# Kernel tuning notes

Measured on AMD Instinct MI355X. Metric: run time of the kernel, lower is better.

The kernel has to match this reference:

```python
import jax, jax.numpy as jnp
import numpy as np

BATCH, IN_DIM, OUT_DIM = 4096, 8192, 16384

# Each of the 16 logic gates is affine in {1, a, b, a*b}. Rows below give the
# coefficients (const, a, b, ab) for gate k, matching the torch `gate` match-case.
_GATE_COEFS = np.array([
    [0, 0, 0, 0],    # 0: zeros
    [0, 0, 0, 1],    # 1: a*b
    [0, 1, 0, -1],   # 2: a - a*b
    [0, 1, 0, 0],    # 3: a
    [0, 0, 1, -1],   # 4: b - a*b
    [0, 0, 1, 0],    # 5: b
    [0, 1, 1, -2],   # 6: a + b - 2ab (xor)
    [0, 1, 1, -1],   # 7: a + b - ab (or)
    [1, -1, -1, 1],  # 8: 1 - (a + b - ab) (nor)
    [1, -1, -1, 2],  # 9: 1 - (a + b - 2ab) (xnor)
    [1, 0, -1, 0],   # 10: 1 - b
    [1, 0, -1, 1],   # 11: 1 - b + ab
    [1, -1, 0, 0],   # 12: 1 - a
    [1, -1, 0, 1],   # 13: 1 - a + ab
    [1, 0, 0, -1],   # 14: 1 - ab (nand)
    [1, 0, 0, 0],    # 15: ones
], dtype=np.float32)


def setup_inputs() -> dict:
    key = jax.random.key(0)
    k1, k2, k3, k4 = jax.random.split(key, 4)
    x = jax.random.uniform(k1, (BATCH, IN_DIM), dtype=jnp.float32)
    weights = jax.random.normal(k2, (OUT_DIM, 16), dtype=jnp.float32)
    idx_a = jax.random.randint(k3, (OUT_DIM,), 0, IN_DIM, dtype=jnp.int32)
    idx_b = jax.random.randint(k4, (OUT_DIM,), 0, IN_DIM, dtype=jnp.int32)
    return {"x": x, "weights": weights, "idx_a": idx_a, "idx_b": idx_b}


def reference(x, weights, idx_a, idx_b):
    # Training path: softmax over the 16 gate logits per output neuron.
    w = jax.nn.softmax(weights, axis=-1)            # [O, 16]
    # Collapse the 16-gate weighted sum into 4 affine coefficients per neuron.
    coef = w @ jnp.asarray(_GATE_COEFS)             # [O, 4] -> (c0, ca, cb, cab)
    a = x[..., idx_a]                               # [B, O] gather
    b = x[..., idx_b]                               # [B, O] gather
    return coef[:, 0] + coef[:, 1] * a + coef[:, 2] * b + coef[:, 3] * (a * b)
```

## Files before the change

kernel.cpp:

```cpp
#include <hip/hip_runtime.h>
#include <cstddef>
#include <cstdint>

constexpr int BATCH   = 4096;
constexpr int IN_DIM  = 8192;
constexpr int OUT_DIM = 16384;
constexpr int THREADS = 512;
constexpr int ROWS    = 8;
constexpr int PAIRS   = ROWS / 2;
constexpr int NBLK    = BATCH / ROWS;
constexpr int OPT     = 4;
constexpr int CHUNKS  = OUT_DIM / (THREADS * OPT);
constexpr int SSTEPS  = (IN_DIM / 4) / THREADS;

typedef float    f32x4 __attribute__((ext_vector_type(4)));
typedef uint32_t u32x4 __attribute__((ext_vector_type(4)));

__device__ __forceinline__ uint32_t f2bf(float f) {
  uint32_t u = __float_as_uint(f);
  u += 0x7fffu + ((u >> 16) & 1u);
  return u >> 16;
}
__device__ __forceinline__ uint32_t pack_bf(float a, float b) {
  return f2bf(a) | (f2bf(b) << 16);
}
__device__ __forceinline__ float bf_lo(uint32_t u) { return __uint_as_float(u << 16); }
__device__ __forceinline__ float bf_hi(uint32_t u) { return __uint_as_float(u & 0xffff0000u); }

__global__ __launch_bounds__(64)
void coef_kernel(const float* __restrict__ weights,
                 const int* __restrict__ idx_a,
                 const int* __restrict__ idx_b,
                 float4* __restrict__ coef,
                 uint32_t* __restrict__ pidx) {
  const int o = blockIdx.x * 64 + threadIdx.x;
  if (o >= OUT_DIM) return;

  const float4* wp = reinterpret_cast<const float4*>(weights + (size_t)o * 16);
  float4 t0 = wp[0], t1 = wp[1], t2 = wp[2], t3 = wp[3];
  float w[16] = { t0.x, t0.y, t0.z, t0.w, t1.x, t1.y, t1.z, t1.w,
                  t2.x, t2.y, t2.z, t2.w, t3.x, t3.y, t3.z, t3.w };
  float m = w[0];
#pragma unroll
  for (int i = 1; i < 16; ++i) m = fmaxf(m, w[i]);
  float p[16]; float s = 0.f;
#pragma unroll
  for (int i = 0; i < 16; ++i) { p[i] = __expf(w[i] - m); s += p[i]; }
  const float inv = 1.0f / s;
  const float GC[16]  = {0,0,0,0, 0,0,0,0, 1,1,1,1, 1,1,1,1};
  const float GA[16]  = {0,0,1,1, 0,0,1,1, -1,-1,0,0, -1,-1,0,0};
  const float GB[16]  = {0,0,0,0, 1,1,1,1, -1,-1,-1,-1, 0,0,0,0};
  const float GAB[16] = {0,1,-1,0, -1,0,-2,-1, 1,2,0,1, 0,1,-1,0};
  float c0 = 0.f, ca = 0.f, cb = 0.f, cab = 0.f;
#pragma unroll
  for (int i = 0; i < 16; ++i) {
    c0 += p[i] * GC[i]; ca += p[i] * GA[i];
    cb += p[i] * GB[i]; cab += p[i] * GAB[i];
  }
  coef[o] = make_float4(c0 * inv, ca * inv, cb * inv, cab * inv);
  pidx[o] = (uint32_t)idx_a[o] | ((uint32_t)idx_b[o] << 16);
}

__device__ __forceinline__ float2 eval2(float4 c, uint32_t ga, uint32_t gb) {
  const float a0 = bf_lo(ga), b0 = bf_lo(gb);
  const float a1 = bf_hi(ga), b1 = bf_hi(gb);
  float2 r;
  r.x = fmaf(fmaf(c.w, a0, c.z), b0, fmaf(c.y, a0, c.x));
  r.y = fmaf(fmaf(c.w, a1, c.z), b1, fmaf(c.y, a1, c.x));
  return r;
}

__global__ __launch_bounds__(THREADS, 4)
void logic_main(const float* __restrict__ x,
                const float4* __restrict__ coef,
                const uint32_t* __restrict__ pidx,
                float* __restrict__ out) {
  __shared__ uint32_t seg0[IN_DIM];
  __shared__ uint32_t seg1[IN_DIM];

  const int t    = threadIdx.x;
  const int row0 = blockIdx.x * ROWS;

  f32x4 la[SSTEPS], lb[SSTEPS];

  {
    const f32x4* __restrict__ rA =
        reinterpret_cast<const f32x4*>(x + (size_t)row0 * IN_DIM);
    const f32x4* __restrict__ rB =
        reinterpret_cast<const f32x4*>(x + (size_t)(row0 + 1) * IN_DIM);
#pragma unroll
    for (int s = 0; s < SSTEPS; ++s) {
      const int q = s * THREADS + t;
      la[s] = rA[q]; lb[s] = rB[q];
    }
#pragma unroll
    for (int s = 0; s < SSTEPS; ++s) {
      const int q = s * THREADS + t;
      u32x4 pk;
      pk.x = pack_bf(la[s].x, lb[s].x);
      pk.y = pack_bf(la[s].y, lb[s].y);
      pk.z = pack_bf(la[s].z, lb[s].z);
      pk.w = pack_bf(la[s].w, lb[s].w);
      *reinterpret_cast<u32x4*>(&seg0[4 * q]) = pk;
    }
  }
  __syncthreads();

  for (int p = 0; p < PAIRS; ++p) {
    const int bLo = row0 + 2 * p;
    const uint32_t* __restrict__ seg = (p & 1) ? seg1 : seg0;
    uint32_t* __restrict__ nxt = (p & 1) ? seg0 : seg1;

    if (p + 1 < PAIRS) {
      const f32x4* __restrict__ rA =
          reinterpret_cast<const f32x4*>(x + (size_t)(bLo + 2) * IN_DIM);
      const f32x4* __restrict__ rB =
          reinterpret_cast<const f32x4*>(x + (size_t)(bLo + 3) * IN_DIM);
#pragma unroll
      for (int s = 0; s < SSTEPS; ++s) {
        const int q = s * THREADS + t;
        la[s] = rA[q]; lb[s] = rB[q];
      }
    }

    {
      int o0 = t * OPT;
      int4   pi = *reinterpret_cast<const int4*>(pidx + o0);
      float4 c0 = coef[o0 + 0], c1 = coef[o0 + 1],
             c2 = coef[o0 + 2], c3 = coef[o0 + 3];

#pragma unroll 2
      for (int ch = 0; ch < CHUNKS; ++ch) {
        const int o = ch * (THREADS * OPT) + t * OPT;

        const uint32_t i0a = (uint32_t)pi.x & 0xffffu, i0b = (uint32_t)pi.x >> 16;
        const uint32_t i1a = (uint32_t)pi.y & 0xffffu, i1b = (uint32_t)pi.y >> 16;
        const uint32_t i2a = (uint32_t)pi.z & 0xffffu, i2b = (uint32_t)pi.z >> 16;
        const uint32_t i3a = (uint32_t)pi.w & 0xffffu, i3b = (uint32_t)pi.w >> 16;

        const uint32_t g0a = seg[i0a], g0b = seg[i0b];
        const uint32_t g1a = seg[i1a], g1b = seg[i1b];
        const uint32_t g2a = seg[i2a], g2b = seg[i2b];
        const uint32_t g3a = seg[i3a], g3b = seg[i3b];

        const float2 e0 = eval2(c0, g0a, g0b);
        const float2 e1 = eval2(c1, g1a, g1b);
        const float2 e2 = eval2(c2, g2a, g2b);
        const float2 e3 = eval2(c3, g3a, g3b);

        f32x4 resLo, resHi;
        resLo.x = e0.x; resLo.y = e1.x; resLo.z = e2.x; resLo.w = e3.x;
        resHi.x = e0.y; resHi.y = e1.y; resHi.z = e2.y; resHi.w = e3.y;

        if (ch + 1 < CHUNKS) {
          const int on = o + THREADS * OPT;
          pi = *reinterpret_cast<const int4*>(pidx + on);
          c0 = coef[on + 0]; c1 = coef[on + 1];
          c2 = coef[on + 2]; c3 = coef[on + 3];
        }

        *reinterpret_cast<f32x4*>(out + (size_t)(bLo + 0) * OUT_DIM + o) = resLo;
        *reinterpret_cast<f32x4*>(out + (size_t)(bLo + 1) * OUT_DIM + o) = resHi;
      }
    }

    if (p + 1 < PAIRS) {
#pragma unroll
      for (int s = 0; s < SSTEPS; ++s) {
        const int q = s * THREADS + t;
        u32x4 pk;
        pk.x = pack_bf(la[s].x, lb[s].x);
        pk.y = pack_bf(la[s].y, lb[s].y);
        pk.z = pack_bf(la[s].z, lb[s].z);
        pk.w = pack_bf(la[s].w, lb[s].w);
        *reinterpret_cast<u32x4*>(&nxt[4 * q]) = pk;
      }
      __syncthreads();
    }
  }
}

extern "C" void kernel_launch(void* const* d_in, const int* in_sizes, int n_in,
                              void* d_out, int out_size, void* d_ws, size_t ws_size,
                              hipStream_t stream) {
  const float* x       = (const float*)d_in[0];
  const float* weights = (const float*)d_in[1];
  const int*   idx_a   = (const int*)d_in[2];
  const int*   idx_b   = (const int*)d_in[3];
  float*       out     = (float*)d_out;

  float4*   coef = (float4*)d_ws;
  uint32_t* pidx = (uint32_t*)((char*)d_ws + (size_t)OUT_DIM * 16);

  coef_kernel<<<OUT_DIM / 64, 64, 0, stream>>>(weights, idx_a, idx_b, coef, pidx);
  logic_main<<<NBLK, THREADS, 0, stream>>>(x, coef, pidx, out);
}
```

Baseline: 102.4 us.

## Process four batch rows per LDS gather with 1024-thread blocks

Each LDS entry now packs four bf16 batch rows (u32x2) instead of two. One gathered index pair then produces four output rows, halving the LDS gather instructions per output and reusing each index/coef load across more rows. Block size doubles to 1024 threads with 16 rows per block, and the chunk loop is fully unrolled with a sched_barrier after the prefetch loads. LDS use doubles to 128 KB per block and register pressure rises, so the number of resident blocks per CU drops.

Measured after the change: 130.2 us. 1.27x slower.

```diff
diff --git a/kernel.cpp b/kernel.cpp
--- a/kernel.cpp
+++ b/kernel.cpp
@@ -5,16 +5,16 @@
 constexpr int BATCH   = 4096;
 constexpr int IN_DIM  = 8192;
 constexpr int OUT_DIM = 16384;
-constexpr int THREADS = 512;
-constexpr int ROWS    = 8;
-constexpr int PAIRS   = ROWS / 2;
+constexpr int THREADS = 1024;
+constexpr int ROWS    = 16;
+constexpr int QUADS   = ROWS / 4;
 constexpr int NBLK    = BATCH / ROWS;
 constexpr int OPT     = 4;
 constexpr int CHUNKS  = OUT_DIM / (THREADS * OPT);
 constexpr int SSTEPS  = (IN_DIM / 4) / THREADS;
 
 typedef float    f32x4 __attribute__((ext_vector_type(4)));
-typedef uint32_t u32x4 __attribute__((ext_vector_type(4)));
+typedef uint32_t u32x2 __attribute__((ext_vector_type(2)));
 
 __device__ __forceinline__ uint32_t f2bf(float f) {
   uint32_t u = __float_as_uint(f);
@@ -75,52 +75,62 @@
                 const float4* __restrict__ coef,
                 const uint32_t* __restrict__ pidx,
                 float* __restrict__ out) {
-  __shared__ uint32_t seg0[IN_DIM];
-  __shared__ uint32_t seg1[IN_DIM];
+  __shared__ u32x2 bufA[IN_DIM];
+  __shared__ u32x2 bufB[IN_DIM];
 
   const int t    = threadIdx.x;
   const int row0 = blockIdx.x * ROWS;
 
-  f32x4 la[SSTEPS], lb[SSTEPS];
+  f32x4 la[SSTEPS], lb[SSTEPS], lc[SSTEPS], ld[SSTEPS];
 
   {
     const f32x4* __restrict__ rA =
-        reinterpret_cast<const f32x4*>(x + (size_t)row0 * IN_DIM);
+        reinterpret_cast<const f32x4*>(x + (size_t)(row0 + 0) * IN_DIM);
     const f32x4* __restrict__ rB =
         reinterpret_cast<const f32x4*>(x + (size_t)(row0 + 1) * IN_DIM);
+    const f32x4* __restrict__ rC =
+        reinterpret_cast<const f32x4*>(x + (size_t)(row0 + 2) * IN_DIM);
+    const f32x4* __restrict__ rD =
+        reinterpret_cast<const f32x4*>(x + (size_t)(row0 + 3) * IN_DIM);
 #pragma unroll
     for (int s = 0; s < SSTEPS; ++s) {
       const int q = s * THREADS + t;
-      la[s] = rA[q]; lb[s] = rB[q];
+      la[s] = rA[q]; lb[s] = rB[q]; lc[s] = rC[q]; ld[s] = rD[q];
     }
 #pragma unroll
     for (int s = 0; s < SSTEPS; ++s) {
       const int q = s * THREADS + t;
-      u32x4 pk;
-      pk.x = pack_bf(la[s].x, lb[s].x);
-      pk.y = pack_bf(la[s].y, lb[s].y);
-      pk.z = pack_bf(la[s].z, lb[s].z);
-      pk.w = pack_bf(la[s].w, lb[s].w);
-      *reinterpret_cast<u32x4*>(&seg0[4 * q]) = pk;
+      u32x2 p0, p1, p2, p3;
+      p0.x = pack_bf(la[s].x, lb[s].x); p0.y = pack_bf(lc[s].x, ld[s].x);
+      p1.x = pack_bf(la[s].y, lb[s].y); p1.y = pack_bf(lc[s].y, ld[s].y);
+      p2.x = pack_bf(la[s].z, lb[s].z); p2.y = pack_bf(lc[s].z, ld[s].z);
+      p3.x = pack_bf(la[s].w, lb[s].w); p3.y = pack_bf(lc[s].w, ld[s].w);
+      bufA[4 * q + 0] = p0; bufA[4 * q + 1] = p1;
+      bufA[4 * q + 2] = p2; bufA[4 * q + 3] = p3;
     }
   }
   __syncthreads();
 
-  for (int p = 0; p < PAIRS; ++p) {
-    const int bLo = row0 + 2 * p;
-    const uint32_t* __restrict__ seg = (p & 1) ? seg1 : seg0;
-    uint32_t* __restrict__ nxt = (p & 1) ? seg0 : seg1;
-
-    if (p + 1 < PAIRS) {
+  for (int qd = 0; qd < QUADS; ++qd) {
+    const int bLo = row0 + 4 * qd;
+    const u32x2* __restrict__ buf = (qd & 1) ? bufB : bufA;
+    u32x2* __restrict__ nxt = (qd & 1) ? bufA : bufB;
+
+    if (qd + 1 < QUADS) {
       const f32x4* __restrict__ rA =
-          reinterpret_cast<const f32x4*>(x + (size_t)(bLo + 2) * IN_DIM);
+          reinterpret_cast<const f32x4*>(x + (size_t)(bLo + 4) * IN_DIM);
       const f32x4* __restrict__ rB =
-          reinterpret_cast<const f32x4*>(x + (size_t)(bLo + 3) * IN_DIM);
+          reinterpret_cast<const f32x4*>(x + (size_t)(bLo + 5) * IN_DIM);
+      const f32x4* __restrict__ rC =
+          reinterpret_cast<const f32x4*>(x + (size_t)(bLo + 6) * IN_DIM);
+      const f32x4* __restrict__ rD =
+          reinterpret_cast<const f32x4*>(x + (size_t)(bLo + 7) * IN_DIM);
 #pragma unroll
       for (int s = 0; s < SSTEPS; ++s) {
         const int q = s * THREADS + t;
-        la[s] = rA[q]; lb[s] = rB[q];
+        la[s] = rA[q]; lb[s] = rB[q]; lc[s] = rC[q]; ld[s] = rD[q];
       }
+      __builtin_amdgcn_sched_barrier(0);
     }
 
     {
@@ -129,7 +139,7 @@
       float4 c0 = coef[o0 + 0], c1 = coef[o0 + 1],
              c2 = coef[o0 + 2], c3 = coef[o0 + 3];
 
-#pragma unroll 2
+#pragma unroll
       for (int ch = 0; ch < CHUNKS; ++ch) {
         const int o = ch * (THREADS * OPT) + t * OPT;
 
@@ -138,19 +148,21 @@
         const uint32_t i2a = (uint32_t)pi.z & 0xffffu, i2b = (uint32_t)pi.z >> 16;
         const uint32_t i3a = (uint32_t)pi.w & 0xffffu, i3b = (uint32_t)pi.w >> 16;
 
-        const uint32_t g0a = seg[i0a], g0b = seg[i0b];
-        const uint32_t g1a = seg[i1a], g1b = seg[i1b];
-        const uint32_t g2a = seg[i2a], g2b = seg[i2b];
-        const uint32_t g3a = seg[i3a], g3b = seg[i3b];
-
-        const float2 e0 = eval2(c0, g0a, g0b);
-        const float2 e1 = eval2(c1, g1a, g1b);
-        const float2 e2 = eval2(c2, g2a, g2b);
-        const float2 e3 = eval2(c3, g3a, g3b);
-
-        f32x4 resLo, resHi;
-        resLo.x = e0.x; resLo.y = e1.x; resLo.z = e2.x; resLo.w = e3.x;
-        resHi.x = e0.y; resHi.y = e1.y; resHi.z = e2.y; resHi.w = e3.y;
+        const u32x2 g0a = buf[i0a], g0b = buf[i0b];
+        const u32x2 g1a = buf[i1a], g1b = buf[i1b];
+        const u32x2 g2a = buf[i2a], g2b = buf[i2b];
+        const u32x2 g3a = buf[i3a], g3b = buf[i3b];
+
+        const float2 e0lo = eval2(c0, g0a.x, g0b.x), e0hi = eval2(c0, g0a.y, g0b.y);
+        const float2 e1lo = eval2(c1, g1a.x, g1b.x), e1hi = eval2(c1, g1a.y, g1b.y);
+        const float2 e2lo = eval2(c2, g2a.x, g2b.x), e2hi = eval2(c2, g2a.y, g2b.y);
+        const float2 e3lo = eval2(c3, g3a.x, g3b.x), e3hi = eval2(c3, g3a.y, g3b.y);
+
+        f32x4 res0, res1, res2, res3;
+        res0.x = e0lo.x; res0.y = e1lo.x; res0.z = e2lo.x; res0.w = e3lo.x;
+        res1.x = e0lo.y; res1.y = e1lo.y; res1.z = e2lo.y; res1.w = e3lo.y;
+        res2.x = e0hi.x; res2.y = e1hi.x; res2.z = e2hi.x; res2.w = e3hi.x;
+        res3.x = e0hi.y; res3.y = e1hi.y; res3.z = e2hi.y; res3.w = e3hi.y;
 
         if (ch + 1 < CHUNKS) {
           const int on = o + THREADS * OPT;
@@ -159,21 +171,24 @@
           c2 = coef[on + 2]; c3 = coef[on + 3];
         }
 
-        *reinterpret_cast<f32x4*>(out + (size_t)(bLo + 0) * OUT_DIM + o) = resLo;
-        *reinterpret_cast<f32x4*>(out + (size_t)(bLo + 1) * OUT_DIM + o) = resHi;
+        *reinterpret_cast<f32x4*>(out + (size_t)(bLo + 0) * OUT_DIM + o) = res0;
+        *reinterpret_cast<f32x4*>(out + (size_t)(bLo + 1) * OUT_DIM + o) = res1;
+        *reinterpret_cast<f32x4*>(out + (size_t)(bLo + 2) * OUT_DIM + o) = res2;
+        *reinterpret_cast<f32x4*>(out + (size_t)(bLo + 3) * OUT_DIM + o) = res3;
       }
     }
 
-    if (p + 1 < PAIRS) {
+    if (qd + 1 < QUADS) {
 #pragma unroll
       for (int s = 0; s < SSTEPS; ++s) {
         const int q = s * THREADS + t;
-        u32x4 pk;
-        pk.x = pack_bf(la[s].x, lb[s].x);
-        pk.y = pack_bf(la[s].y, lb[s].y);
-        pk.z = pack_bf(la[s].z, lb[s].z);
-        pk.w = pack_bf(la[s].w, lb[s].w);
-        *reinterpret_cast<u32x4*>(&nxt[4 * q]) = pk;
+        u32x2 p0, p1, p2, p3;
+        p0.x = pack_bf(la[s].x, lb[s].x); p0.y = pack_bf(lc[s].x, ld[s].x);
+        p1.x = pack_bf(la[s].y, lb[s].y); p1.y = pack_bf(lc[s].y, ld[s].y);
+        p2.x = pack_bf(la[s].z, lb[s].z); p2.y = pack_bf(lc[s].z, ld[s].z);
+        p3.x = pack_bf(la[s].w, lb[s].w); p3.y = pack_bf(lc[s].w, ld[s].w);
+        nxt[4 * q + 0] = p0; nxt[4 * q + 1] = p1;
+        nxt[4 * q + 2] = p2; nxt[4 * q + 3] = p3;
       }
       __syncthreads();
     }
```
